# Kernel tuning notes

Hardware: AMD Instinct MI355X
Metric: run time of the kernel (lower is better)

## Reference

```python
import jax, jax.numpy as jnp
import numpy as np
import math

ETA = 0.01
SIG = 5.0


def _conv2d(x, w, b, pad):
    # x: (B, Cin, H, W), w: (Cout, Cin, kh, kw)
    y = jax.lax.conv_general_dilated(
        x, w, window_strides=(1, 1), padding=[(pad, pad), (pad, pad)],
        dimension_numbers=('NCHW', 'OIHW', 'NCHW'))
    return y + b[None, :, None, None]


def _sim_flow(x, corr_w, corr_b):
    # x: (N, C, T, H, W)
    N, C, T, H, W = x.shape
    Tp = T - 1
    # correspond_conv: ReLU -> 1x1x1 Conv3d (C -> C//2)
    tm = jnp.einsum('oc,ncthw->nothw', corr_w, jax.nn.relu(x)) + corr_b[None, :, None, None, None]
    tm = tm.transpose(0, 2, 1, 3, 4)  # (N, T, C//2, H, W)
    bh = tm[:, 1:]   # (N, Tp, Cp, H, W)
    bf = tm[:, :-1]
    # full correlation volume: (N, Tp, H, W, H, W); (a,b)=bh coords, (u,v)=bf coords
    score = jnp.einsum('ntcab,ntcuv->ntabuv', bh, bf)
    flat = score.reshape(N, Tp, H * W, H, W)
    max_score = flat.max(axis=2, keepdims=True)             # (N, Tp, 1, H, W)
    inds = jnp.argmax(flat, axis=2)[:, :, None]             # (N, Tp, 1, H, W)
    idx_x = (inds // H).astype(score.dtype)                 # faithful: // H as in source
    idx_y = (inds % H).astype(score.dtype)
    px = jnp.arange(H, dtype=score.dtype).reshape(1, 1, H, 1, 1)
    py = jnp.arange(W, dtype=score.dtype).reshape(1, 1, W, 1, 1)
    norm = math.sqrt(2.0 * math.pi) * SIG
    g_x = jnp.exp((px - idx_x) / (SIG ** 2)) / norm         # (N, Tp, H, H, W)
    g_y = jnp.exp((py - idx_y) / (SIG ** 2)) / norm         # (N, Tp, W, H, W)
    score_x = (g_x[:, :, :, None, :, :] * score).reshape(N, Tp, H * W, H, W)
    coef_x = jax.nn.softmax(score_x / ETA, axis=2)
    score_y = (g_y[:, :, None, :, :, :] * score).reshape(N, Tp, H * W, H, W)
    coef_y = jax.nn.softmax(score_y / ETA, axis=2)
    epx = jnp.repeat(jnp.arange(H, dtype=score.dtype), W).reshape(1, 1, H * W, 1, 1)
    epy = jnp.tile(jnp.arange(W, dtype=score.dtype), H).reshape(1, 1, H * W, 1, 1)
    d_x = (epx * coef_x).sum(axis=2, keepdims=True)         # (N, Tp, 1, H, W)
    d_y = (epy * coef_y).sum(axis=2, keepdims=True)
    return jnp.concatenate([d_x, d_y, max_score], axis=2)   # (N, Tp, 3, H, W)


def setup_inputs() -> dict:
    key = jax.random.key(0)
    ks = jax.random.split(key, 8)
    N, C, T, H, W = 4, 256, 8, 28, 28
    Cp = C // 2
    s = 0.05
    return {
        'input_tem_map': jax.random.normal(ks[0], (N, C, T, H, W), jnp.float32),
        'corr_w': jax.random.normal(ks[1], (Cp, C), jnp.float32) * s,
        'corr_b': jnp.zeros((Cp,), jnp.float32),
        'mw1': jax.random.normal(ks[2], (64, 3, 5, 5), jnp.float32) * s,
        'mb1': jnp.zeros((64,), jnp.float32),
        'mw2': jax.random.normal(ks[3], (128, 64, 3, 3), jnp.float32) * s,
        'mb2': jnp.zeros((128,), jnp.float32),
        'mw3': jax.random.normal(ks[4], (Cp, 128, 3, 3), jnp.float32) * s,
        'mb3': jnp.zeros((Cp,), jnp.float32),
        'mw4': jax.random.normal(ks[5], (C, Cp, 3, 3), jnp.float32) * s,
        'mb4': jnp.zeros((C,), jnp.float32),
        'lin_w': jax.random.normal(ks[6], (C, C), jnp.float32) * s,
        'lin_b': jnp.zeros((C,), jnp.float32),
    }


def reference(input_tem_map, corr_w, corr_b, mw1, mb1, mw2, mb2, mw3, mb3, mw4, mb4, lin_w, lin_b):
    x = input_tem_map
    N, C, T, H, W = x.shape
    Tp = T - 1
    y = x.mean(axis=(2, 3, 4))                               # appearance vector (N, C)
    sim = _sim_flow(x, corr_w, corr_b)                       # (N, Tp, 3, H, W)
    # motion_conv: all time kernels are 1 -> fold Tp into batch and use 2D convs
    m = jax.nn.relu(sim).reshape(N * Tp, 3, H, W)
    m = jax.nn.relu(_conv2d(m, mw1, mb1, 1))                 # k5 pad1 -> (H-2, W-2)
    m = jax.nn.relu(_conv2d(m, mw2, mb2, 1))
    m = jax.nn.relu(_conv2d(m, mw3, mb3, 1))
    m = _conv2d(m, mw4, mb4, 1)                              # (N*Tp, C, H-2, W-2)
    motion_vec = m.reshape(N, Tp, C, H - 2, W - 2).mean(axis=(1, 3, 4))  # (N, C)
    z = jax.nn.relu(y + motion_vec) @ lin_w.T + lin_b        # W = ReLU -> Linear
    return z
```

## Files before the change

kernel.cpp:

```cpp
#include <hip/hip_runtime.h>


#define NORM_INV 0.07978845608028654f

typedef __attribute__((ext_vector_type(8))) short bf16x8;
typedef __attribute__((ext_vector_type(4))) float f32x4;

__device__ inline ushort f2bf(float v) {
  union { float f; uint u; } c; c.f = v;
  const uint u = c.u + 0x7FFFu + ((c.u >> 16) & 1u);
  return (ushort)(u >> 16);
}
__device__ inline float bf2f(ushort h) {
  union { uint u; float f; } c; c.u = ((uint)h) << 16;
  return c.f;
}

__device__ __forceinline__ void glds16(const void* g, void* l) {
  __builtin_amdgcn_global_load_lds(
      (const __attribute__((address_space(1))) void*)g,
      (__attribute__((address_space(3))) void*)l, 16, 0, 0);
}

__device__ __forceinline__ void pack_w_one(const float* __restrict__ w,
    ushort* __restrict__ Bp, int CIN, int N16, int idx) {
  const int j = idx & 7;
  const int l = (idx >> 3) & 63;
  const int rest = idx >> 9;
  const int n16 = rest % N16;
  const int kc = rest / N16;
  const int co = n16 * 16 + (l & 15);
  const int kk = kc * 32 + (l >> 4) * 8 + j;
  const int tap = kk / CIN;
  const int ci = kk - tap * CIN;
  Bp[idx] = f2bf(w[((size_t)co * CIN + ci) * 9 + tap]);
}

__global__ __launch_bounds__(256) void pack_all_kernel(
    const float* __restrict__ cw, const float* __restrict__ mw2,
    const float* __restrict__ mw3, const float* __restrict__ mw4,
    ushort* __restrict__ bph, ushort* __restrict__ bpl,
    ushort* __restrict__ bp2, ushort* __restrict__ bp3,
    ushort* __restrict__ bp4, float* __restrict__ y) {
  int idx = blockIdx.x * 256 + threadIdx.x;
  if (idx < 32768) {
    const int j = idx & 7, l = (idx >> 3) & 63, rest = idx >> 9;
    const int n16 = rest & 7, kc = rest >> 3;
    const int co = n16 * 16 + (l & 15);
    const int k = kc * 32 + (l >> 4) * 8 + j;
    const float v = cw[co * 256 + k];
    const ushort h = f2bf(v);
    bph[idx] = h;
    bpl[idx] = f2bf(v - bf2f(h));
    return;
  }
  idx -= 32768;
  if (idx < 73728)  { pack_w_one(mw2, bp2, 64, 8, idx);  return; }
  idx -= 73728;
  if (idx < 147456) { pack_w_one(mw3, bp3, 128, 8, idx); return; }
  idx -= 147456;
  if (idx < 294912) { pack_w_one(mw4, bp4, 128, 16, idx); return; }
  idx -= 294912;
  if (idx < 1024) y[idx] = 0.f;
}

__global__ __launch_bounds__(256) void xb_kernel(const float* __restrict__ x,
    ushort* __restrict__ xh, ushort* __restrict__ xl, float* __restrict__ y) {
  const int tid = threadIdx.x;
  const int p0 = blockIdx.x * 64;
  const int c0 = blockIdx.y * 64;
  const int nt = blockIdx.z;
  const int n = nt >> 3, t = nt & 7;
  __shared__ float tile[64][65];
  const float* xp = x + (((size_t)n * 256 + c0) * 8 + t) * 784;
#pragma unroll
  for (int i = 0; i < 4; ++i) {
    const int idx = i * 256 + tid;
    const int c = idx >> 4, q = idx & 15;
    const int hw = p0 + q * 4;
    const float* sp = xp + (size_t)c * 6272 + hw;
    if (hw + 3 < 784) {
      const float4 v = *(const float4*)sp;
      tile[q * 4 + 0][c] = v.x; tile[q * 4 + 1][c] = v.y;
      tile[q * 4 + 2][c] = v.z; tile[q * 4 + 3][c] = v.w;
    } else {
#pragma unroll
      for (int e = 0; e < 4; ++e)
        tile[q * 4 + e][c] = (hw + e < 784) ? sp[e] : 0.f;
    }
  }
  __syncthreads();
#pragma unroll
  for (int i = 0; i < 8; ++i) {
    const int idx = i * 256 + tid;
    const int p = idx >> 5, c2 = (idx & 31) * 2;
    const int hw = p0 + p;
    if (hw < 784) {
      const size_t o = ((size_t)nt * 784 + hw) * 256 + c0 + c2;
      const float v0 = fmaxf(tile[p][c2], 0.f);
      const float v1 = fmaxf(tile[p][c2 + 1], 0.f);
      const ushort h0 = f2bf(v0), h1 = f2bf(v1);
      ushort2 hv, lv;
      hv.x = h0; hv.y = h1;
      lv.x = f2bf(v0 - bf2f(h0)); lv.y = f2bf(v1 - bf2f(h1));
      *(ushort2*)(xh + o) = hv;
      *(ushort2*)(xl + o) = lv;
    }
  }
  if (tid < 64) {
    float s = 0.f;
#pragma unroll 8
    for (int p = 0; p < 64; ++p) s += tile[p][tid];
    atomicAdd(y + n * 256 + c0 + tid, s);
  }
}

__global__ __launch_bounds__(256) void tm_gemm_kernel(
    const ushort* __restrict__ xh, const ushort* __restrict__ xl,
    const ushort* __restrict__ bph, const ushort* __restrict__ bpl,
    const float* __restrict__ cb, ushort* __restrict__ tmt) {
  const int tid = threadIdx.x;
  const int w = tid >> 6, l = tid & 63;
  const int lr = l & 15, lq = l >> 4;
  const int mtile = blockIdx.x * 4 + w;
  const int ntile = blockIdx.y;
  const size_t r0 = (size_t)(mtile * 32 + lr) * 256 + lq * 8;
  const size_t r1 = r0 + 16 * 256;
  f32x4 acc[2][2];
#pragma unroll
  for (int mf = 0; mf < 2; ++mf)
#pragma unroll
    for (int nf = 0; nf < 2; ++nf) { f32x4 z = {0.f,0.f,0.f,0.f}; acc[mf][nf] = z; }
#pragma unroll
  for (int kc = 0; kc < 8; ++kc) {
    const bf16x8 ah0 = *(const bf16x8*)(xh + r0 + kc * 32);
    const bf16x8 ah1 = *(const bf16x8*)(xh + r1 + kc * 32);
    const bf16x8 al0 = *(const bf16x8*)(xl + r0 + kc * 32);
    const bf16x8 al1 = *(const bf16x8*)(xl + r1 + kc * 32);
    const size_t bo = ((size_t)(kc * 8 + ntile * 2) * 64 + l) * 8;
    const bf16x8 bh0 = *(const bf16x8*)(bph + bo);
    const bf16x8 bh1 = *(const bf16x8*)(bph + bo + 512);
    const bf16x8 bl0 = *(const bf16x8*)(bpl + bo);
    const bf16x8 bl1 = *(const bf16x8*)(bpl + bo + 512);
    acc[0][0] = __builtin_amdgcn_mfma_f32_16x16x32_bf16(ah0, bh0, acc[0][0], 0,0,0);
    acc[0][1] = __builtin_amdgcn_mfma_f32_16x16x32_bf16(ah0, bh1, acc[0][1], 0,0,0);
    acc[1][0] = __builtin_amdgcn_mfma_f32_16x16x32_bf16(ah1, bh0, acc[1][0], 0,0,0);
    acc[1][1] = __builtin_amdgcn_mfma_f32_16x16x32_bf16(ah1, bh1, acc[1][1], 0,0,0);
    acc[0][0] = __builtin_amdgcn_mfma_f32_16x16x32_bf16(al0, bh0, acc[0][0], 0,0,0);
    acc[0][1] = __builtin_amdgcn_mfma_f32_16x16x32_bf16(al0, bh1, acc[0][1], 0,0,0);
    acc[1][0] = __builtin_amdgcn_mfma_f32_16x16x32_bf16(al1, bh0, acc[1][0], 0,0,0);
    acc[1][1] = __builtin_amdgcn_mfma_f32_16x16x32_bf16(al1, bh1, acc[1][1], 0,0,0);
    acc[0][0] = __builtin_amdgcn_mfma_f32_16x16x32_bf16(ah0, bl0, acc[0][0], 0,0,0);
    acc[0][1] = __builtin_amdgcn_mfma_f32_16x16x32_bf16(ah0, bl1, acc[0][1], 0,0,0);
    acc[1][0] = __builtin_amdgcn_mfma_f32_16x16x32_bf16(ah1, bl0, acc[1][0], 0,0,0);
    acc[1][1] = __builtin_amdgcn_mfma_f32_16x16x32_bf16(ah1, bl1, acc[1][1], 0,0,0);
  }
#pragma unroll
  for (int nf = 0; nf < 2; ++nf) {
    const int co = ntile * 32 + nf * 16 + lr;
    const float bv = cb[co];
#pragma unroll
    for (int mf = 0; mf < 2; ++mf)
#pragma unroll
      for (int r = 0; r < 4; ++r) {
        const int pix = mtile * 32 + mf * 16 + lq * 4 + r;
        tmt[(size_t)pix * 128 + co] = f2bf(acc[mf][nf][r] + bv);
      }
  }
}

__global__ __launch_bounds__(512) void score_kernel(const ushort* __restrict__ tmt,
    float* __restrict__ m0) {
  const int tid = threadIdx.x;
  const int nt = blockIdx.y;
  const int n = nt / 7, t = nt % 7;
  const int uv0 = blockIdx.x * 16;
  const ushort* bfp = tmt + (size_t)(n * 8 + t) * 784 * 128;
  const ushort* bhp = tmt + (size_t)(n * 8 + t + 1) * 784 * 128;
  __shared__ float sc[16 * 785];
  __shared__ float gt[16 * 64];
  const int w = tid >> 6;
  const int l = tid & 63;
  const int lr = l & 15, lq = l >> 4;
  bf16x8 af[4];
#pragma unroll
  for (int kc = 0; kc < 4; ++kc)
    af[kc] = *(const bf16x8*)(bfp + (uv0 + lr) * 128 + kc * 32 + lq * 8);
  f32x4 acc[7];
#pragma unroll
  for (int i = 0; i < 7; ++i) { f32x4 z = {0.f,0.f,0.f,0.f}; acc[i] = z; }
#pragma unroll
  for (int i = 0; i < 7; ++i) {
    const int nf = i * 8 + w;
    if (nf < 49) {
      const ushort* bp = bhp + (nf * 16 + lr) * 128 + lq * 8;
      const bf16x8 b0 = *(const bf16x8*)(bp);
      const bf16x8 b1 = *(const bf16x8*)(bp + 32);
      const bf16x8 b2 = *(const bf16x8*)(bp + 64);
      const bf16x8 b3 = *(const bf16x8*)(bp + 96);
      acc[i] = __builtin_amdgcn_mfma_f32_16x16x32_bf16(af[0], b0, acc[i], 0,0,0);
      acc[i] = __builtin_amdgcn_mfma_f32_16x16x32_bf16(af[1], b1, acc[i], 0,0,0);
      acc[i] = __builtin_amdgcn_mfma_f32_16x16x32_bf16(af[2], b2, acc[i], 0,0,0);
      acc[i] = __builtin_amdgcn_mfma_f32_16x16x32_bf16(af[3], b3, acc[i], 0,0,0);
    }
  }
#pragma unroll
  for (int i = 0; i < 7; ++i) {
    const int nf = i * 8 + w;
    if (nf < 49) {
#pragma unroll
      for (int r = 0; r < 4; ++r)
        sc[(lq * 4 + r) * 785 + nf * 16 + lr] = acc[i][r];
    }
  }
  __syncthreads();
  const int row = tid >> 5, l32 = tid & 31;
  const float* rowp = &sc[row * 785];
  float bv = -1e30f; int bi = 0;
#pragma unroll 5
  for (int i = 0; i < 25; ++i) {
    const int a2 = i * 32 + l32;
    if (a2 < 784) {
      const float v = rowp[a2];
      if (v > bv) { bv = v; bi = a2; }
    }
  }
#pragma unroll
  for (int off = 16; off; off >>= 1) {
    const float ov = __shfl_xor(bv, off, 32);
    const int oi = __shfl_xor(bi, off, 32);
    if (ov > bv || (ov == bv && oi < bi)) { bv = ov; bi = oi; }
  }
  const int ast = bi / 28;
  const int bst = bi - ast * 28;
  float* g = &gt[row * 64];
  if (l32 < 28) {
    g[l32]      = __expf((float)(l32 - ast) * 0.04f) * NORM_INV;
    g[32 + l32] = __expf((float)(l32 - bst) * 0.04f) * NORM_INV;
  }
  float mx = -1e30f, my = -1e30f;
#pragma unroll 5
  for (int i = 0; i < 25; ++i) {
    const int a2 = i * 32 + l32;
    if (a2 < 784) {
      const float v = rowp[a2];
      const int a = a2 / 28; const int bb = a2 - a * 28;
      mx = fmaxf(mx, g[a] * v); my = fmaxf(my, g[32 + bb] * v);
    }
  }
#pragma unroll
  for (int off = 16; off; off >>= 1) {
    mx = fmaxf(mx, __shfl_xor(mx, off, 32));
    my = fmaxf(my, __shfl_xor(my, off, 32));
  }
  float sx = 0.f, sxw = 0.f, sy = 0.f, syw = 0.f;
#pragma unroll 5
  for (int i = 0; i < 25; ++i) {
    const int a2 = i * 32 + l32;
    if (a2 < 784) {
      const float v = rowp[a2];
      const int a = a2 / 28; const int bb = a2 - a * 28;
      const float ex = __expf((g[a] * v - mx) * 100.f);
      const float ey = __expf((g[32 + bb] * v - my) * 100.f);
      sx += ex; sxw += (float)a * ex;
      sy += ey; syw += (float)bb * ey;
    }
  }
#pragma unroll
  for (int off = 16; off; off >>= 1) {
    sx += __shfl_xor(sx, off, 32); sxw += __shfl_xor(sxw, off, 32);
    sy += __shfl_xor(sy, off, 32); syw += __shfl_xor(syw, off, 32);
  }
  if (l32 == 0) {
    const int uv = uv0 + row;
    float* op = m0 + (size_t)nt * 3 * 784 + uv;
    op[0]    = fmaxf(sxw / sx, 0.f);
    op[784]  = fmaxf(syw / sy, 0.f);
    op[1568] = fmaxf(bv, 0.f);
  }
}

__global__ __launch_bounds__(256) void border_zero_kernel(
    ushort* __restrict__ m1, ushort* __restrict__ m2, ushort* __restrict__ m3) {
  const int idx = blockIdx.x * 256 + threadIdx.x;
  if (idx >= 28 * 108 * 40) return;
  const int c = idx % 40;
  const int rest = idx / 40;
  const int bp = rest % 108;
  const int b = rest / 108;
  int ipo;
  if (bp < 28) ipo = bp;
  else if (bp < 56) ipo = 756 + (bp - 28);
  else {
    const int r = 1 + (bp - 56) / 2;
    ipo = r * 28 + ((bp - 56) & 1) * 27;
  }
  const bf16x8 z = {0,0,0,0,0,0,0,0};
  if (c < 8)       *(bf16x8*)(m1 + ((size_t)b * 784 + ipo) * 64  + c * 8) = z;
  else if (c < 24) *(bf16x8*)(m2 + ((size_t)b * 784 + ipo) * 128 + (c - 8) * 8) = z;
  else             *(bf16x8*)(m3 + ((size_t)b * 784 + ipo) * 128 + (c - 24) * 8) = z;
}

__global__ __launch_bounds__(256) void conv1_kernel(const float* __restrict__ m0,
    const float* __restrict__ w, const float* __restrict__ bias,
    ushort* __restrict__ out) {
  const int b = blockIdx.z;
  const int pg = blockIdx.y;
  const int co0 = blockIdx.x * 16;
  const int tid = threadIdx.x;
  __shared__ float il[3 * 784];
  __shared__ float wl[75 * 16];
  const float* ip = m0 + (size_t)b * 2352;
  for (int i = tid; i < 2352; i += 256) il[i] = ip[i];
  for (int i = tid; i < 1200; i += 256) {
    const int c = i & 15, rest = i >> 4;
    wl[i] = w[(size_t)(co0 + c) * 75 + rest];
  }
  __syncthreads();
  const int pix = pg * 256 + tid;
  if (pix >= 676) return;
  const int py = pix / 26, px = pix - py * 26;
  float acc[16];
#pragma unroll
  for (int c = 0; c < 16; ++c) acc[c] = 0.f;
  for (int ci = 0; ci < 3; ++ci) {
#pragma unroll
    for (int dy = 0; dy < 5; ++dy) {
      const int iy = py + dy - 1;
      if ((unsigned)iy >= 28u) continue;
#pragma unroll
      for (int dx = 0; dx < 5; ++dx) {
        const int ix = px + dx - 1;
        if ((unsigned)ix >= 28u) continue;
        const float v = il[ci * 784 + iy * 28 + ix];
        const float* wp = &wl[(ci * 25 + dy * 5 + dx) * 16];
#pragma unroll
        for (int c4 = 0; c4 < 16; c4 += 4) {
          const float4 wv = *(const float4*)&wp[c4];
          acc[c4 + 0] += wv.x * v; acc[c4 + 1] += wv.y * v;
          acc[c4 + 2] += wv.z * v; acc[c4 + 3] += wv.w * v;
        }
      }
    }
  }
  const int ipo = (py + 1) * 28 + px + 1;
  ushort* op = out + ((size_t)b * 784 + ipo) * 64 + co0;
#pragma unroll
  for (int c = 0; c < 16; ++c)
    op[c] = f2bf(fmaxf(acc[c] + bias[co0 + c], 0.f));
}

template<int CIN, int COUT, int BM, bool FINAL>
__global__ __launch_bounds__(256) void conv_lds_kernel(
    const ushort* __restrict__ in, const ushort* __restrict__ Bp,
    const float* __restrict__ bias, ushort* __restrict__ outp,
    float* __restrict__ outf) {
  constexpr int KC = CIN * 9 / 32;
  constexpr int CPG = CIN / 32;
  constexpr int N16 = COUT / 16;
  constexpr int MF = BM / 32;
  constexpr int PA = BM / 64;
  constexpr int ABYTES = BM * 64;
  __shared__ __align__(16) char lds[2 * ABYTES + 16384];
  const int tid = threadIdx.x;
  const int w = tid >> 6, l = tid & 63;
  const int wm = w >> 1, wn = w & 1;
  const int lr = l & 15, lq = l >> 4;
  const int mt = blockIdx.x, nt = blockIdx.y;

  size_t srcA[PA];
#pragma unroll
  for (int p = 0; p < PA; ++p) {
    const int e = p * 256 + tid;
    const int P = e % BM, kq = e / BM;
    int GP = mt * BM + P;
    if (GP > 18927) GP = 18927;
    const int b = GP / 676, pp = GP - b * 676;
    const int ipb = pp + 2 * (pp / 26);
    srcA[p] = ((size_t)b * 784 + ipb) * CIN + kq * 8;
  }

  auto stage = [&](int kc, int buf) {
    const int tap = kc / CPG;
    const int ktoff = ((tap / 3) * 28 + (tap - (tap / 3) * 3)) * CIN +
                      (kc - tap * CPG) * 32;
#pragma unroll
    for (int p = 0; p < PA; ++p)
      glds16(in + srcA[p] + ktoff,
             lds + buf * ABYTES + p * 4096 + w * 1024);
    const ushort* bsrc = Bp + ((size_t)kc * N16 + nt * 8) * 512;
#pragma unroll
    for (int p = 0; p < 2; ++p)
      glds16(bsrc + p * 2048 + tid * 8,
             lds + 2 * ABYTES + buf * 8192 + p * 4096 + w * 1024);
  };

  f32x4 acc[MF][4];
#pragma unroll
  for (int mf = 0; mf < MF; ++mf)
#pragma unroll
    for (int nf = 0; nf < 4; ++nf) { f32x4 z = {0.f,0.f,0.f,0.f}; acc[mf][nf] = z; }

  stage(0, 0);
  __syncthreads();
  int buf = 0;
  for (int kc = 0; kc < KC; ++kc) {
    if (kc + 1 < KC) stage(kc + 1, buf ^ 1);
    const char* Ab = lds + buf * ABYTES;
    const char* Bb = lds + 2 * ABYTES + buf * 8192;
    bf16x8 afr[MF], bfr[4];
#pragma unroll
    for (int mf = 0; mf < MF; ++mf)
      afr[mf] = *(const bf16x8*)(Ab + lq * (BM * 16) +
                                 (wm * (BM / 2) + mf * 16 + lr) * 16);
#pragma unroll
    for (int nf = 0; nf < 4; ++nf)
      bfr[nf] = *(const bf16x8*)(Bb + ((wn * 4 + nf) * 64 + l) * 16);
#pragma unroll
    for (int mf = 0; mf < MF; ++mf)
#pragma unroll
      for (int nf = 0; nf < 4; ++nf)
        acc[mf][nf] = __builtin_amdgcn_mfma_f32_16x16x32_bf16(
            afr[mf], bfr[nf], acc[mf][nf], 0, 0, 0);
    __syncthreads();
    buf ^= 1;
  }

#pragma unroll
  for (int nf = 0; nf < 4; ++nf) {
    const int co = nt * 128 + wn * 64 + nf * 16 + lr;
    const float bvv = bias[co];
#pragma unroll
    for (int mf = 0; mf < MF; ++mf) {
#pragma unroll
      for (int r = 0; r < 4; ++r) {
        const int P = mt * BM + wm * (BM / 2) + mf * 16 + lq * 4 + r;
        if (P < 18928) {
          const int b = P / 676, pp = P - b * 676;
          const float v = acc[mf][nf][r] + bvv;
          if constexpr (FINAL) {
            outf[((size_t)b * COUT + co) * 676 + pp] = v;
          } else {
            const int ipo = pp + 2 * (pp / 26) + 29;
            outp[((size_t)b * 784 + ipo) * COUT + co] = f2bf(fmaxf(v, 0.f));
          }
        }
      }
    }
  }
}

__global__ __launch_bounds__(256) void final_reduce_kernel(
    const float* __restrict__ y, const float* __restrict__ m4,
    float* __restrict__ r) {
  const int nc = blockIdx.x;
  const int n = nc >> 8, c = nc & 255;
  const int tid = threadIdx.x;
  float s2 = 0.f;
  for (int t = 0; t < 7; ++t) {
    const float* ms = m4 + ((size_t)(n * 7 + t) * 256 + c) * 676;
    for (int i = tid; i < 676; i += 256) s2 += ms[i];
  }
#pragma unroll
  for (int off = 32; off; off >>= 1) s2 += __shfl_down(s2, off);
  __shared__ float red[4];
  if ((tid & 63) == 0) red[tid >> 6] = s2;
  __syncthreads();
  if (tid == 0) {
    const float tot = red[0] + red[1] + red[2] + red[3];
    r[nc] = fmaxf(y[nc] * (1.f / 6272.f) + tot * (1.f / 4732.f), 0.f);
  }
}

__global__ __launch_bounds__(256) void linear_kernel(const float* __restrict__ r,
    const float* __restrict__ lw, const float* __restrict__ lb,
    float* __restrict__ out) {
  const int n = blockIdx.x;
  const int j = threadIdx.x;
  __shared__ float rl[256];
  rl[j] = r[n * 256 + j];
  __syncthreads();
  float acc = lb[j];
  const float* w = lw + (size_t)j * 256;
#pragma unroll 4
  for (int c = 0; c < 256; c += 4) {
    const float4 wv = *(const float4*)&w[c];
    acc += wv.x * rl[c] + wv.y * rl[c + 1] + wv.z * rl[c + 2] + wv.w * rl[c + 3];
  }
  out[n * 256 + j] = acc;
}

extern "C" void kernel_launch(void* const* d_in, const int* in_sizes, int n_in,
                              void* d_out, int out_size, void* d_ws, size_t ws_size,
                              hipStream_t stream) {
  const float* x      = (const float*)d_in[0];
  const float* corr_w = (const float*)d_in[1];
  const float* corr_b = (const float*)d_in[2];
  const float* mw1 = (const float*)d_in[3];
  const float* mb1 = (const float*)d_in[4];
  const float* mw2 = (const float*)d_in[5];
  const float* mb2 = (const float*)d_in[6];
  const float* mw3 = (const float*)d_in[7];
  const float* mb3 = (const float*)d_in[8];
  const float* mw4 = (const float*)d_in[9];
  const float* mb4 = (const float*)d_in[10];
  const float* lin_w = (const float*)d_in[11];
  const float* lin_b = (const float*)d_in[12];
  float* out = (float*)d_out;
  char* wsb = (char*)d_ws;

  ushort* xh  = (ushort*)(wsb + 0);
  ushort* xl  = (ushort*)(wsb + 12845056);
  ushort* tmt = (ushort*)(wsb + 25690112);
  float*  m4  = (float*)(wsb + 0);
  ushort* m1  = (ushort*)(wsb + 19382272);
  ushort* m2  = (ushort*)(wsb + 22192128);
  ushort* m3  = (ushort*)(wsb + 27811840);
  float*  m0  = (float*)(wsb + 33431552);
  float*  rr  = (float*)(wsb + 33694976);
  ushort* Bp2 = (ushort*)(wsb + 33699072);
  ushort* Bp3 = (ushort*)(wsb + 33846528);
  ushort* Bp4 = (ushort*)(wsb + 34141440);
  ushort* Bph = (ushort*)(wsb + 34731264);
  ushort* Bpl = (ushort*)(wsb + 34796800);
  float*  y   = (float*)(wsb + 34862336);

  pack_all_kernel<<<dim3(2148), 256, 0, stream>>>(
      corr_w, mw2, mw3, mw4, Bph, Bpl, Bp2, Bp3, Bp4, y);

  xb_kernel<<<dim3(13, 4, 32), 256, 0, stream>>>(x, xh, xl, y);
  tm_gemm_kernel<<<dim3(196, 4), 256, 0, stream>>>(xh, xl, Bph, Bpl, corr_b, tmt);
  score_kernel<<<dim3(49, 28), 512, 0, stream>>>(tmt, m0);

  border_zero_kernel<<<dim3(473), 256, 0, stream>>>(m1, m2, m3);

  conv1_kernel<<<dim3(4, 3, 28), 256, 0, stream>>>(m0, mw1, mb1, m1);
  conv_lds_kernel<64, 128, 64, false><<<dim3(296, 1), 256, 0, stream>>>(
      m1, Bp2, mb2, m2, nullptr);
  conv_lds_kernel<128, 128, 64, false><<<dim3(296, 1), 256, 0, stream>>>(
      m2, Bp3, mb3, m3, nullptr);
  conv_lds_kernel<128, 256, 128, true><<<dim3(148, 2), 256, 0, stream>>>(
      m3, Bp4, mb4, nullptr, m4);
  final_reduce_kernel<<<dim3(1024), 256, 0, stream>>>(y, m4, rr);
  linear_kernel<<<dim3(4), 256, 0, stream>>>(rr, lin_w, lin_b, out);
}
```

Baseline: 288.9 us.

## Retile channel GEMM to full N per wave and restructure score softmax loops

The tm GEMM now gives each wave a 16-row M tile covering all 128 output channels, so each A fragment is loaded once and reused across 8 N tiles, instead of a 2x2 tile spread over 4 N blocks. The score kernel is reorganised so each lane owns one column (b) of the 28x28 score map. This makes the y-Gaussian weight constant per lane: the y-max comes from the per-lane max already found, and the y-weighted sum becomes l32*sy. It also drops the per-element divide/modulo. The trade-offs are more B traffic per wave and more accumulator registers in the GEMM, and four idle lanes per 32 in the score loops.

```diff
diff --git a/kernel.cpp b/kernel.cpp
--- a/kernel.cpp
+++ b/kernel.cpp
@@ -123,49 +123,33 @@
   const int w = tid >> 6, l = tid & 63;
   const int lr = l & 15, lq = l >> 4;
   const int mtile = blockIdx.x * 4 + w;
-  const int ntile = blockIdx.y;
-  const size_t r0 = (size_t)(mtile * 32 + lr) * 256 + lq * 8;
-  const size_t r1 = r0 + 16 * 256;
-  f32x4 acc[2][2];
-#pragma unroll
-  for (int mf = 0; mf < 2; ++mf)
-#pragma unroll
-    for (int nf = 0; nf < 2; ++nf) { f32x4 z = {0.f,0.f,0.f,0.f}; acc[mf][nf] = z; }
+  const size_t r0 = (size_t)(mtile * 16 + lr) * 256 + lq * 8;
+  f32x4 acc[8];
+#pragma unroll
+  for (int i = 0; i < 8; ++i) { f32x4 z = {0.f,0.f,0.f,0.f}; acc[i] = z; }
 #pragma unroll
   for (int kc = 0; kc < 8; ++kc) {
-    const bf16x8 ah0 = *(const bf16x8*)(xh + r0 + kc * 32);
-    const bf16x8 ah1 = *(const bf16x8*)(xh + r1 + kc * 32);
-    const bf16x8 al0 = *(const bf16x8*)(xl + r0 + kc * 32);
-    const bf16x8 al1 = *(const bf16x8*)(xl + r1 + kc * 32);
-    const size_t bo = ((size_t)(kc * 8 + ntile * 2) * 64 + l) * 8;
-    const bf16x8 bh0 = *(const bf16x8*)(bph + bo);
-    const bf16x8 bh1 = *(const bf16x8*)(bph + bo + 512);
-    const bf16x8 bl0 = *(const bf16x8*)(bpl + bo);
-    const bf16x8 bl1 = *(const bf16x8*)(bpl + bo + 512);
-    acc[0][0] = __builtin_amdgcn_mfma_f32_16x16x32_bf16(ah0, bh0, acc[0][0], 0,0,0);
-    acc[0][1] = __builtin_amdgcn_mfma_f32_16x16x32_bf16(ah0, bh1, acc[0][1], 0,0,0);
-    acc[1][0] = __builtin_amdgcn_mfma_f32_16x16x32_bf16(ah1, bh0, acc[1][0], 0,0,0);
-    acc[1][1] = __builtin_amdgcn_mfma_f32_16x16x32_bf16(ah1, bh1, acc[1][1], 0,0,0);
-    acc[0][0] = __builtin_amdgcn_mfma_f32_16x16x32_bf16(al0, bh0, acc[0][0], 0,0,0);
-    acc[0][1] = __builtin_amdgcn_mfma_f32_16x16x32_bf16(al0, bh1, acc[0][1], 0,0,0);
-    acc[1][0] = __builtin_amdgcn_mfma_f32_16x16x32_bf16(al1, bh0, acc[1][0], 0,0,0);
-    acc[1][1] = __builtin_amdgcn_mfma_f32_16x16x32_bf16(al1, bh1, acc[1][1], 0,0,0);
-    acc[0][0] = __builtin_amdgcn_mfma_f32_16x16x32_bf16(ah0, bl0, acc[0][0], 0,0,0);
-    acc[0][1] = __builtin_amdgcn_mfma_f32_16x16x32_bf16(ah0, bl1, acc[0][1], 0,0,0);
-    acc[1][0] = __builtin_amdgcn_mfma_f32_16x16x32_bf16(ah1, bl0, acc[1][0], 0,0,0);
-    acc[1][1] = __builtin_amdgcn_mfma_f32_16x16x32_bf16(ah1, bl1, acc[1][1], 0,0,0);
-  }
-#pragma unroll
-  for (int nf = 0; nf < 2; ++nf) {
-    const int co = ntile * 32 + nf * 16 + lr;
+    const bf16x8 ah = *(const bf16x8*)(xh + r0 + kc * 32);
+    const bf16x8 al = *(const bf16x8*)(xl + r0 + kc * 32);
+#pragma unroll
+    for (int n16 = 0; n16 < 8; ++n16) {
+      const size_t bo = ((size_t)(kc * 8 + n16) * 64 + l) * 8;
+      const bf16x8 bh = *(const bf16x8*)(bph + bo);
+      const bf16x8 bl = *(const bf16x8*)(bpl + bo);
+      acc[n16] = __builtin_amdgcn_mfma_f32_16x16x32_bf16(ah, bh, acc[n16], 0,0,0);
+      acc[n16] = __builtin_amdgcn_mfma_f32_16x16x32_bf16(al, bh, acc[n16], 0,0,0);
+      acc[n16] = __builtin_amdgcn_mfma_f32_16x16x32_bf16(ah, bl, acc[n16], 0,0,0);
+    }
+  }
+#pragma unroll
+  for (int n16 = 0; n16 < 8; ++n16) {
+    const int co = n16 * 16 + lr;
     const float bv = cb[co];
 #pragma unroll
-    for (int mf = 0; mf < 2; ++mf)
-#pragma unroll
-      for (int r = 0; r < 4; ++r) {
-        const int pix = mtile * 32 + mf * 16 + lq * 4 + r;
-        tmt[(size_t)pix * 128 + co] = f2bf(acc[mf][nf][r] + bv);
-      }
+    for (int r = 0; r < 4; ++r) {
+      const int pix = mtile * 16 + lq * 4 + r;
+      tmt[(size_t)pix * 128 + co] = f2bf(acc[n16][r] + bv);
+    }
   }
 }
 
@@ -178,7 +162,7 @@
   const ushort* bfp = tmt + (size_t)(n * 8 + t) * 784 * 128;
   const ushort* bhp = tmt + (size_t)(n * 8 + t + 1) * 784 * 128;
   __shared__ float sc[16 * 785];
-  __shared__ float gt[16 * 64];
+  __shared__ float gxs[16][28];
   const int w = tid >> 6;
   const int l = tid & 63;
   const int lr = l & 15, lq = l >> 4;
@@ -215,16 +199,17 @@
   }
   __syncthreads();
   const int row = tid >> 5, l32 = tid & 31;
+  const bool act = l32 < 28;
   const float* rowp = &sc[row * 785];
-  float bv = -1e30f; int bi = 0;
-#pragma unroll 5
-  for (int i = 0; i < 25; ++i) {
-    const int a2 = i * 32 + l32;
-    if (a2 < 784) {
-      const float v = rowp[a2];
-      if (v > bv) { bv = v; bi = a2; }
-    }
-  }
+  float bv = -1e30f; int bi = 1 << 20;
+#pragma unroll
+  for (int a = 0; a < 28; ++a) {
+    if (act) {
+      const float v = rowp[a * 28 + l32];
+      if (v > bv) { bv = v; bi = a * 28 + l32; }
+    }
+  }
+  const float bvp = bv;
 #pragma unroll
   for (int off = 16; off; off >>= 1) {
     const float ov = __shfl_xor(bv, off, 32);
@@ -233,39 +218,31 @@
   }
   const int ast = bi / 28;
   const int bst = bi - ast * 28;
-  float* g = &gt[row * 64];
-  if (l32 < 28) {
-    g[l32]      = __expf((float)(l32 - ast) * 0.04f) * NORM_INV;
-    g[32 + l32] = __expf((float)(l32 - bst) * 0.04f) * NORM_INV;
-  }
-  float mx = -1e30f, my = -1e30f;
-#pragma unroll 5
-  for (int i = 0; i < 25; ++i) {
-    const int a2 = i * 32 + l32;
-    if (a2 < 784) {
-      const float v = rowp[a2];
-      const int a = a2 / 28; const int bb = a2 - a * 28;
-      mx = fmaxf(mx, g[a] * v); my = fmaxf(my, g[32 + bb] * v);
-    }
-  }
+  if (act) gxs[row][l32] = __expf((float)(l32 - ast) * 0.04f) * NORM_INV;
+  const float gy = __expf((float)(l32 - bst) * 0.04f) * NORM_INV;
+  float mx = -1e30f;
+#pragma unroll
+  for (int a = 0; a < 28; ++a) {
+    if (act) mx = fmaxf(mx, gxs[row][a] * rowp[a * 28 + l32]);
+  }
+  float my = act ? gy * bvp : -1e30f;
 #pragma unroll
   for (int off = 16; off; off >>= 1) {
     mx = fmaxf(mx, __shfl_xor(mx, off, 32));
     my = fmaxf(my, __shfl_xor(my, off, 32));
   }
-  float sx = 0.f, sxw = 0.f, sy = 0.f, syw = 0.f;
-#pragma unroll 5
-  for (int i = 0; i < 25; ++i) {
-    const int a2 = i * 32 + l32;
-    if (a2 < 784) {
-      const float v = rowp[a2];
-      const int a = a2 / 28; const int bb = a2 - a * 28;
-      const float ex = __expf((g[a] * v - mx) * 100.f);
-      const float ey = __expf((g[32 + bb] * v - my) * 100.f);
+  float sx = 0.f, sxw = 0.f, sy = 0.f;
+#pragma unroll
+  for (int a = 0; a < 28; ++a) {
+    if (act) {
+      const float v = rowp[a * 28 + l32];
+      const float ex = __expf((gxs[row][a] * v - mx) * 100.f);
+      const float ey = __expf((gy * v - my) * 100.f);
       sx += ex; sxw += (float)a * ex;
-      sy += ey; syw += (float)bb * ey;
-    }
-  }
+      sy += ey;
+    }
+  }
+  float syw = (float)l32 * sy;
 #pragma unroll
   for (int off = 16; off; off >>= 1) {
     sx += __shfl_xor(sx, off, 32); sxw += __shfl_xor(sxw, off, 32);
@@ -529,7 +506,7 @@
       corr_w, mw2, mw3, mw4, Bph, Bpl, Bp2, Bp3, Bp4, y);
 
   xb_kernel<<<dim3(13, 4, 32), 256, 0, stream>>>(x, xh, xl, y);
-  tm_gemm_kernel<<<dim3(196, 4), 256, 0, stream>>>(xh, xl, Bph, Bpl, corr_b, tmt);
+  tm_gemm_kernel<<<dim3(392), 256, 0, stream>>>(xh, xl, Bph, Bpl, corr_b, tmt);
   score_kernel<<<dim3(49, 28), 512, 0, stream>>>(tmt, m0);
 
   border_zero_kernel<<<dim3(473), 256, 0, stream>>>(m1, m2, m3);
```

New measurement: 280.1 us. 3.0% less time.
